# Kernel tuning notes

Measured on AMD Instinct MI355X. Metric: run time of the kernel, lower is better.

Reference implementation:

```python
import jax, jax.numpy as jnp
import numpy as np

B, L = 4, 1024
D_IN, D_MODEL, DEPTH = 8, 512, 4
D_INNER, D_STATE, D_CONV = 2 * D_MODEL, 16, 4
DT_RANK = (D_MODEL + 15) // 16  # 32


def setup_inputs():
    key = jax.random.key(0)
    ks = jax.random.split(key, 12)
    s = 0.02
    inp = {
        "x": jax.random.normal(ks[0], (B, L, D_IN), jnp.float32),
        "in_w": jax.random.normal(ks[1], (D_MODEL, D_IN), jnp.float32) * s,
        "in_b": jnp.zeros((D_MODEL,), jnp.float32),
        "W_xz": jax.random.normal(ks[2], (DEPTH, 2 * D_INNER, D_MODEL), jnp.float32) * s,
        "conv_w": jax.random.normal(ks[3], (DEPTH, D_INNER, D_CONV), jnp.float32) * 0.1,
        "conv_b": jnp.zeros((DEPTH, D_INNER), jnp.float32),
        "W_xp": jax.random.normal(ks[4], (DEPTH, DT_RANK + 2 * D_STATE, D_INNER), jnp.float32) * s,
        "W_dt": jax.random.normal(ks[5], (DEPTH, D_INNER, DT_RANK), jnp.float32) * 0.1,
        "b_dt": jax.random.uniform(ks[6], (DEPTH, D_INNER), jnp.float32, -4.0, -2.0),
        "A_log": jnp.broadcast_to(jnp.log(jnp.arange(1, D_STATE + 1, dtype=jnp.float32)), (DEPTH, D_INNER, D_STATE)) + 0.0,
        "D_param": jnp.ones((DEPTH, D_INNER), jnp.float32),
        "W_out": jax.random.normal(ks[7], (DEPTH, D_MODEL, D_INNER), jnp.float32) * s,
        "ln_g": jnp.ones((D_MODEL,), jnp.float32),
        "ln_b": jnp.zeros((D_MODEL,), jnp.float32),
    }
    return inp


def _silu(x):
    return x * jax.nn.sigmoid(x)


def _mamba_layer(h, Wxz, cw, cb, Wxp, Wdt, bdt, A_log, Dp, Wout):
    # in_proj -> (x, z)
    xz = jnp.einsum('bld,ed->ble', h, Wxz)           # (B,L,2*D_INNER)
    xc, z = jnp.split(xz, 2, axis=-1)
    # causal depthwise conv1d, kernel D_CONV
    xp = jnp.pad(xc, ((0, 0), (D_CONV - 1, 0), (0, 0)))
    xconv = sum(xp[:, k:k + L, :] * cw[:, k] for k in range(D_CONV)) + cb
    u = _silu(xconv)                                 # (B,L,D_INNER)
    # x_proj -> dt, B, C
    xdbl = jnp.einsum('bld,ed->ble', u, Wxp)
    dt_lr = xdbl[..., :DT_RANK]
    Bm = xdbl[..., DT_RANK:DT_RANK + D_STATE]        # (B,L,D_STATE)
    Cm = xdbl[..., DT_RANK + D_STATE:]               # (B,L,D_STATE)
    dt = jax.nn.softplus(jnp.einsum('blr,dr->bld', dt_lr, Wdt) + bdt)  # (B,L,D_INNER)
    A = -jnp.exp(A_log)                              # (D_INNER,D_STATE)

    def step(hst, inp):
        dt_t, B_t, C_t, u_t = inp                    # (B,Di),(B,S),(B,S),(B,Di)
        dA = jnp.exp(dt_t[..., None] * A)            # (B,Di,S)
        dBu = dt_t[..., None] * B_t[:, None, :] * u_t[..., None]
        hst = dA * hst + dBu
        y_t = jnp.einsum('bds,bs->bd', hst, C_t)
        return hst, y_t

    h0 = jnp.zeros((h.shape[0], D_INNER, D_STATE), h.dtype)
    xs = (dt.transpose(1, 0, 2), Bm.transpose(1, 0, 2), Cm.transpose(1, 0, 2), u.transpose(1, 0, 2))
    _, ys = jax.lax.scan(step, h0, xs)
    y = ys.transpose(1, 0, 2) + u * Dp               # (B,L,D_INNER)
    y = y * _silu(z)
    return jnp.einsum('ble,de->bld', y, Wout)


def reference(x, in_w, in_b, W_xz, conv_w, conv_b, W_xp, W_dt, b_dt, A_log, D_param, W_out, ln_g, ln_b):
    h = jnp.einsum('bli,di->bld', x, in_w) + in_b
    for i in range(DEPTH):
        h = _mamba_layer(h, W_xz[i], conv_w[i], conv_b[i], W_xp[i], W_dt[i], b_dt[i], A_log[i], D_param[i], W_out[i])
    mu = h.mean(-1, keepdims=True)
    var = ((h - mu) ** 2).mean(-1, keepdims=True)
    return (h - mu) * jax.lax.rsqrt(var + 1e-5) * ln_g + ln_b
```

## Files before the change

### kernel.cpp

```cpp
#include <hip/hip_runtime.h>
#include <math.h>

#define B_      4
#define L_      1024
#define D_INNC  8
#define DMODEL  512
#define DEPTH_  4
#define DINNER  1024
#define DSTATE  16
#define DCONV   4
#define DTRANK  32
#define MTOT    (B_*L_)
#define CHUNKS  32
#define CLEN    32

typedef float f32x4 __attribute__((ext_vector_type(4)));
typedef short s16x8 __attribute__((ext_vector_type(8)));
typedef unsigned short u16;
typedef unsigned short u16x4v __attribute__((ext_vector_type(4)));

__device__ __forceinline__ u16 f2bf(float v) {
    unsigned b = __float_as_uint(v);
    return (u16)((b + 0x7FFF + ((b >> 16) & 1)) >> 16);
}
__device__ __forceinline__ float bf2f(u16 h) {
    return __uint_as_float((unsigned)h << 16);
}

__global__ __launch_bounds__(256) void in_proj_kernel(
    const float* __restrict__ x, const float* __restrict__ w,
    const float* __restrict__ bias, u16* __restrict__ hb)
{
    int idx = blockIdx.x * 256 + threadIdx.x;
    int m = idx / DMODEL, d = idx % DMODEL;
    const float* xr = x + m * D_INNC;
    const float* wr = w + d * D_INNC;
    float acc = bias[d];
#pragma unroll
    for (int k = 0; k < D_INNC; ++k) acc += xr[k] * wr[k];
    hb[idx] = f2bf(acc);
}

__global__ __launch_bounds__(256) void wconv_kernel(
    const float* __restrict__ W, u16* __restrict__ Wb)
{
    int i = blockIdx.x * 256 + threadIdx.x;
    const float* src = W + (size_t)i * 8;
    float4 f0 = *(const float4*)src;
    float4 f1 = *(const float4*)(src + 4);
    float f[8] = {f0.x,f0.y,f0.z,f0.w,f1.x,f1.y,f1.z,f1.w};
    s16x8 hv;
#pragma unroll
    for (int e = 0; e < 8; ++e) hv[e] = (short)f2bf(f[e]);
    *(s16x8*)(Wb + (size_t)i * 8) = hv;
}

template<int BM, int BN, int MODE>
__global__ __launch_bounds__(256, 2) void gemm_bf16(
    const u16* __restrict__ A, int lda,
    const u16* __restrict__ B, int ldb,
    void* __restrict__ C0, void* __restrict__ C1,
    int ldc, int K)
{
    constexpr int FM  = BM / 32;
    constexpr int FN  = BN / 32;
    constexpr int ACH = BM / 64;
    constexpr int BCH = BN / 64;
    __shared__ __align__(16) u16 As[4*(BM+1)*8];
    __shared__ __align__(16) u16 Bs[4*(BN+1)*8];

    const int t    = threadIdx.x;
    const int lane = t & 63;
    const int w    = t >> 6;
    const int wm   = (w >> 1) * (BM / 2);
    const int wn   = (w & 1) * (BN / 2);
    const int quad = lane >> 4;
    const int l16  = lane & 15;
    const int m0   = blockIdx.y * BM;
    const int n0   = blockIdx.x * BN;

    f32x4 acc[FM][FN];
#pragma unroll
    for (int i = 0; i < FM; ++i)
#pragma unroll
        for (int j = 0; j < FN; ++j) acc[i][j] = (f32x4){0.f,0.f,0.f,0.f};

    s16x8 ra[ACH], rb[BCH];
#pragma unroll
    for (int c = 0; c < ACH; ++c) {
        int id = c*256 + t, row = id >> 2, kb = id & 3;
        ra[c] = *(const s16x8*)(A + (size_t)(m0 + row) * lda + kb*8);
    }
#pragma unroll
    for (int c = 0; c < BCH; ++c) {
        int id = c*256 + t, row = id >> 2, kb = id & 3;
        rb[c] = *(const s16x8*)(B + (size_t)(n0 + row) * ldb + kb*8);
    }

    for (int kk = 0; kk < K; kk += 32) {
        __syncthreads();
#pragma unroll
        for (int c = 0; c < ACH; ++c) {
            int id = c*256 + t, row = id >> 2, kb = id & 3;
            *(s16x8*)&As[(kb*(BM+1) + row) * 8] = ra[c];
        }
#pragma unroll
        for (int c = 0; c < BCH; ++c) {
            int id = c*256 + t, row = id >> 2, kb = id & 3;
            *(s16x8*)&Bs[(kb*(BN+1) + row) * 8] = rb[c];
        }
        __syncthreads();
        int kn = kk + 32;
        if (kn < K) {
#pragma unroll
            for (int c = 0; c < ACH; ++c) {
                int id = c*256 + t, row = id >> 2, kb = id & 3;
                ra[c] = *(const s16x8*)(A + (size_t)(m0 + row) * lda + kn + kb*8);
            }
#pragma unroll
            for (int c = 0; c < BCH; ++c) {
                int id = c*256 + t, row = id >> 2, kb = id & 3;
                rb[c] = *(const s16x8*)(B + (size_t)(n0 + row) * ldb + kn + kb*8);
            }
        }
        s16x8 afr[FM], bfr[FN];
#pragma unroll
        for (int i = 0; i < FM; ++i)
            afr[i] = *(const s16x8*)&As[(quad*(BM+1) + wm + i*16 + l16) * 8];
#pragma unroll
        for (int j = 0; j < FN; ++j)
            bfr[j] = *(const s16x8*)&Bs[(quad*(BN+1) + wn + j*16 + l16) * 8];
#pragma unroll
        for (int i = 0; i < FM; ++i)
#pragma unroll
            for (int j = 0; j < FN; ++j)
                acc[i][j] = __builtin_amdgcn_mfma_f32_16x16x32_bf16(afr[i], bfr[j], acc[i][j], 0, 0, 0);
    }

    if (MODE == 2) {
        u16* C = (u16*)C0;
#pragma unroll
        for (int i = 0; i < FM; ++i)
#pragma unroll
            for (int j = 0; j < FN; ++j) {
                int col = n0 + wn + j*16 + l16;
#pragma unroll
                for (int r = 0; r < 4; ++r) {
                    int row = m0 + wm + i*16 + quad*4 + r;
                    C[(size_t)row * ldc + col] = f2bf(acc[i][j][r]);
                }
            }
    } else if (MODE == 3) {
        u16*  dtlr = (u16*)C0;
        float* xd  = (float*)C1;
#pragma unroll
        for (int i = 0; i < FM; ++i)
#pragma unroll
            for (int j = 0; j < FN; ++j) {
                int col = n0 + wn + j*16 + l16;
#pragma unroll
                for (int r = 0; r < 4; ++r) {
                    int row = m0 + wm + i*16 + quad*4 + r;
                    float v = acc[i][j][r];
                    if (col < 32) dtlr[(size_t)row * 32 + col] = f2bf(v);
                    else          xd[(size_t)row * 64 + col]   = v;
                }
            }
    } else if (MODE == 4) {
        u16* dtb_ = (u16*)C0;
        const float* bdt = (const float*)C1;
#pragma unroll
        for (int i = 0; i < FM; ++i)
#pragma unroll
            for (int j = 0; j < FN; ++j) {
                int col = n0 + wn + j*16 + l16;
                float bb = bdt[col];
#pragma unroll
                for (int r = 0; r < 4; ++r) {
                    int row = m0 + wm + i*16 + quad*4 + r;
                    float v = acc[i][j][r] + bb;
                    float sp = (v > 20.f) ? v : log1pf(__expf(v));
                    dtb_[(size_t)row * ldc + col] = f2bf(sp);
                }
            }
    } else {
        u16* xcb = (u16*)C0;
        u16* szb = (u16*)C1;
#pragma unroll
        for (int i = 0; i < FM; ++i)
#pragma unroll
            for (int j = 0; j < FN; ++j) {
                int col = n0 + wn + j*16 + l16;
                bool isz = col >= DINNER;
                int cc = col & (DINNER - 1);
                u16* dst = isz ? szb : xcb;
#pragma unroll
                for (int r = 0; r < 4; ++r) {
                    int row = m0 + wm + i*16 + quad*4 + r;
                    float v = acc[i][j][r];
                    if (isz) v = v / (1.f + __expf(-v));
                    dst[(size_t)row * DINNER + cc] = f2bf(v);
                }
            }
    }
}

__global__ __launch_bounds__(256) void conv_silu_kernel(
    const u16* __restrict__ xcb, const float* __restrict__ cw,
    const float* __restrict__ cb, u16* __restrict__ ub)
{
    int idx = (blockIdx.x * 256 + threadIdx.x) * 2;
    int m = idx >> 10;
    int d = idx & (DINNER - 1);
    int l = m & (L_ - 1);

    const float4 w0 = *(const float4*)&cw[d * 4];
    const float4 w1 = *(const float4*)&cw[(d + 1) * 4];
    float a0 = cb[d], a1 = cb[d + 1];
#pragma unroll
    for (int k = 0; k < 4; ++k) {
        int lag = 3 - k;
        if (l >= lag) {
            unsigned v = *(const unsigned*)&xcb[(size_t)(m - lag) * DINNER + d];
            float x0 = bf2f((u16)(v & 0xffff));
            float x1 = bf2f((u16)(v >> 16));
            float wk0 = (&w0.x)[k], wk1 = (&w1.x)[k];
            a0 += x0 * wk0; a1 += x1 * wk1;
        }
    }
    a0 = a0 / (1.f + __expf(-a0));
    a1 = a1 / (1.f + __expf(-a1));
    unsigned pack = (unsigned)f2bf(a0) | ((unsigned)f2bf(a1) << 16);
    *(unsigned*)&ub[idx] = pack;
}

__global__ __launch_bounds__(256) void scan1_kernel(
    const u16* __restrict__ ub, const float* xdbl,
    const u16* __restrict__ dtb, const float* __restrict__ A_log,
    u16* __restrict__ hfinal, float* dtsum_out)
{
    __shared__ float Bs[CLEN][16];
    const int blk  = blockIdx.x;
    const int dblk = blk & 3;
    const int c    = (blk >> 2) & (CHUNKS - 1);
    const int b    = blk >> 7;
    const int d    = dblk * 256 + threadIdx.x;
    const int mbase = b * L_ + c * CLEN;

#pragma unroll
    for (int q = 0; q < 2; ++q) {
        int idx = q * 256 + threadIdx.x;
        int tt = idx >> 4, ss = idx & 15;
        Bs[tt][ss] = xdbl[(size_t)(mbase + tt) * 64 + 32 + ss];
    }
    float A[16];
    {
        float4 a4[4];
#pragma unroll
        for (int q = 0; q < 4; ++q) a4[q] = *(const float4*)&A_log[d * 16 + q * 4];
        const float* af = (const float*)a4;
#pragma unroll
        for (int s = 0; s < 16; ++s) A[s] = -__expf(af[s]);
    }
    __syncthreads();

    float h[16];
#pragma unroll
    for (int s = 0; s < 16; ++s) h[s] = 0.f;
    float dts = 0.f;

    for (int t0 = 0; t0 < CLEN; t0 += 8) {
        float dt8[8], u8[8];
#pragma unroll
        for (int j = 0; j < 8; ++j) {
            int m = mbase + t0 + j;
            dt8[j] = bf2f(dtb[(size_t)m * DINNER + d]);
            u8[j]  = bf2f(ub [(size_t)m * DINNER + d]);
        }
#pragma unroll
        for (int j = 0; j < 8; ++j) {
            float dtv = dt8[j], dtu = dtv * u8[j];
            dts += dtv;
            float Bt[16];
#pragma unroll
            for (int q = 0; q < 4; ++q)
                *(float4*)&Bt[q*4] = *(const float4*)&Bs[t0 + j][q*4];
#pragma unroll
            for (int s = 0; s < 16; ++s) {
                float dA = __expf(dtv * A[s]);
                h[s] = dA * h[s] + dtu * Bt[s];
            }
        }
    }
    size_t base = ((size_t)(b * CHUNKS + c) * DINNER + d) * 16;
    s16x8 p0, p1;
#pragma unroll
    for (int s = 0; s < 8; ++s) { p0[s] = (short)f2bf(h[s]); p1[s] = (short)f2bf(h[s+8]); }
    *(s16x8*)&hfinal[base]     = p0;
    *(s16x8*)&hfinal[base + 8] = p1;
    int i = (b * CHUNKS + c) * DINNER + d;
    dtsum_out[(i >> 5) * 64 + (i & 31)] = dts;
}

__global__ __launch_bounds__(256) void scan2_kernel(
    u16* __restrict__ hfinal, const float* __restrict__ dtsum,
    const float* __restrict__ A_log)
{
    int t = blockIdx.x * 256 + threadIdx.x;
    int s = t & 15, d = (t >> 4) & (DINNER - 1), b = t >> 14;
    float As = -__expf(A_log[d * DSTATE + s]);
    float h = 0.f;
    for (int c0 = 0; c0 < CHUNKS; c0 += 8) {
        float hf8[8], dts8[8];
#pragma unroll
        for (int j = 0; j < 8; ++j) {
            int c = c0 + j;
            int i = (b * CHUNKS + c) * DINNER + d;
            dts8[j] = dtsum[(i >> 5) * 64 + (i & 31)];
            hf8[j]  = bf2f(hfinal[((size_t)i) * 16 + s]);
        }
#pragma unroll
        for (int j = 0; j < 8; ++j) {
            int c = c0 + j;
            size_t idx = ((size_t)((b * CHUNKS + c) * DINNER + d)) * 16 + s;
            hfinal[idx] = f2bf(h);
            h = __expf(As * dts8[j]) * h + hf8[j];
        }
    }
}

__global__ __launch_bounds__(256) void scan3_kernel(
    const u16* __restrict__ szb, const u16* __restrict__ ub,
    const float* xdbl, const u16* __restrict__ dtb,
    const float* __restrict__ A_log, const float* __restrict__ Dp,
    const u16* __restrict__ hstart, u16* __restrict__ yb)
{
    __shared__ float Bs[CLEN][16];
    __shared__ float Cs[CLEN][16];
    const int blk  = blockIdx.x;
    const int dblk = blk & 3;
    const int c    = (blk >> 2) & (CHUNKS - 1);
    const int b    = blk >> 7;
    const int d    = dblk * 256 + threadIdx.x;
    const int mbase = b * L_ + c * CLEN;

#pragma unroll
    for (int q = 0; q < 2; ++q) {
        int idx = q * 256 + threadIdx.x;
        int tt = idx >> 4, ss = idx & 15;
        Bs[tt][ss] = xdbl[(size_t)(mbase + tt) * 64 + 32 + ss];
        Cs[tt][ss] = xdbl[(size_t)(mbase + tt) * 64 + 48 + ss];
    }
    float A[16];
    {
        float4 a4[4];
#pragma unroll
        for (int q = 0; q < 4; ++q) a4[q] = *(const float4*)&A_log[d * 16 + q * 4];
        const float* af = (const float*)a4;
#pragma unroll
        for (int s = 0; s < 16; ++s) A[s] = -__expf(af[s]);
    }
    const float Dval = Dp[d];

    float h[16];
    {
        size_t base = ((size_t)(b * CHUNKS + c) * DINNER + d) * 16;
        s16x8 p0 = *(const s16x8*)&hstart[base];
        s16x8 p1 = *(const s16x8*)&hstart[base + 8];
#pragma unroll
        for (int s = 0; s < 8; ++s) { h[s] = bf2f((u16)p0[s]); h[s+8] = bf2f((u16)p1[s]); }
    }
    __syncthreads();

    for (int t0 = 0; t0 < CLEN; t0 += 8) {
        float dt8[8], u8[8], sz8[8];
#pragma unroll
        for (int j = 0; j < 8; ++j) {
            int m = mbase + t0 + j;
            dt8[j] = bf2f(dtb[(size_t)m * DINNER + d]);
            u8[j]  = bf2f(ub [(size_t)m * DINNER + d]);
            sz8[j] = bf2f(szb[(size_t)m * DINNER + d]);
        }
#pragma unroll
        for (int j = 0; j < 8; ++j) {
            float dtv = dt8[j], dtu = dtv * u8[j];
            float Bt[16], Ct[16];
#pragma unroll
            for (int q = 0; q < 4; ++q) {
                *(float4*)&Bt[q*4] = *(const float4*)&Bs[t0 + j][q*4];
                *(float4*)&Ct[q*4] = *(const float4*)&Cs[t0 + j][q*4];
            }
            float yv = 0.f;
#pragma unroll
            for (int s = 0; s < 16; ++s) {
                float dA = __expf(dtv * A[s]);
                h[s] = dA * h[s] + dtu * Bt[s];
                yv += h[s] * Ct[s];
            }
            int m = mbase + t0 + j;
            yb[(size_t)m * DINNER + d] = f2bf((yv + u8[j] * Dval) * sz8[j]);
        }
    }
}

__global__ __launch_bounds__(256) void ln_kernel(
    const u16* __restrict__ hb, const float* __restrict__ g,
    const float* __restrict__ bta, float* __restrict__ out)
{
    int m = blockIdx.x;
    size_t base = (size_t)m * DMODEL;
    int t = threadIdx.x;
    float v0 = bf2f(hb[base + t]);
    float v1 = bf2f(hb[base + t + 256]);
    float sum = v0 + v1, sq = v0*v0 + v1*v1;
#pragma unroll
    for (int off = 32; off; off >>= 1) {
        sum += __shfl_down(sum, off);
        sq  += __shfl_down(sq,  off);
    }
    __shared__ float ls[4], lq[4];
    int w = t >> 6;
    if ((t & 63) == 0) { ls[w] = sum; lq[w] = sq; }
    __syncthreads();
    sum = ls[0] + ls[1] + ls[2] + ls[3];
    sq  = lq[0] + lq[1] + lq[2] + lq[3];
    float mu  = sum * (1.f / DMODEL);
    float var = sq * (1.f / DMODEL) - mu * mu;
    float rs  = rsqrtf(var + 1e-5f);
    out[base + t]       = (v0 - mu) * rs * g[t]       + bta[t];
    out[base + t + 256] = (v1 - mu) * rs * g[t + 256] + bta[t + 256];
}

extern "C" void kernel_launch(void* const* d_in, const int* in_sizes, int n_in,
                              void* d_out, int out_size, void* d_ws, size_t ws_size,
                              hipStream_t stream)
{
    const float* x      = (const float*)d_in[0];
    const float* in_w   = (const float*)d_in[1];
    const float* in_b   = (const float*)d_in[2];
    const float* W_xz   = (const float*)d_in[3];
    const float* conv_w = (const float*)d_in[4];
    const float* conv_b = (const float*)d_in[5];
    const float* W_xp   = (const float*)d_in[6];
    const float* W_dt   = (const float*)d_in[7];
    const float* b_dt   = (const float*)d_in[8];
    const float* A_log  = (const float*)d_in[9];
    const float* D_par  = (const float*)d_in[10];
    const float* W_out  = (const float*)d_in[11];
    const float* ln_g   = (const float*)d_in[12];
    const float* ln_b   = (const float*)d_in[13];
    float* out = (float*)d_out;

    float* ws      = (float*)d_ws;
    float* hbF     = ws;
    float* hfinF   = hbF    + 1048576;
    float* xcbF    = hfinF  + 1048576;
    float* szbF    = xcbF   + 2097152;
    float* ubF     = szbF   + 2097152;
    float* xdbl    = ubF    + 2097152;
    float* dtbF    = xdbl   + 262144;
    float* ybF     = dtbF   + 2097152;
    float* wxzF    = ybF    + 2097152;
    float* woutF   = wxzF   + 2097152;
    float* wxpF    = woutF  + 1048576;
    float* wdtF    = wxpF   + 131072;
    float* dtlrF   = wdtF   + 65536;

    u16* hb     = (u16*)hbF;
    u16* hfinal = (u16*)hfinF;
    u16* xcb  = (u16*)xcbF;
    u16* szb  = (u16*)szbF;
    u16* ub   = (u16*)ubF;
    u16* dtb  = (u16*)dtbF;
    u16* yb   = (u16*)ybF;
    u16* wxzb  = (u16*)wxzF;
    u16* woutb = (u16*)woutF;
    u16* wxpb  = (u16*)wxpF;
    u16* wdtb  = (u16*)wdtF;
    u16* dtlrb = (u16*)dtlrF;

    wconv_kernel<<<(DEPTH_*2048*DMODEL/8)/256, 256, 0, stream>>>(W_xz, wxzb);
    wconv_kernel<<<(DEPTH_*DMODEL*DINNER/8)/256, 256, 0, stream>>>(W_out, woutb);
    wconv_kernel<<<(DEPTH_*64*DINNER/8)/256, 256, 0, stream>>>(W_xp, wxpb);
    wconv_kernel<<<(DEPTH_*DINNER*DTRANK/8)/256, 256, 0, stream>>>(W_dt, wdtb);

    in_proj_kernel<<<MTOT*DMODEL/256, 256, 0, stream>>>(x, in_w, in_b, hb);

    for (int layer = 0; layer < DEPTH_; ++layer) {
        const float* cw    = conv_w + (size_t)layer * DINNER * DCONV;
        const float* cb    = conv_b + (size_t)layer * DINNER;
        const float* bdt   = b_dt   + (size_t)layer * DINNER;
        const float* Alog  = A_log  + (size_t)layer * DINNER * DSTATE;
        const float* Dp    = D_par  + (size_t)layer * DINNER;
        const u16* wxzL    = wxzb  + (size_t)layer * 2048 * DMODEL;
        const u16* woutL   = woutb + (size_t)layer * DMODEL * DINNER;
        const u16* wxpL    = wxpb  + (size_t)layer * 64 * DINNER;
        const u16* wdtL    = wdtb  + (size_t)layer * DINNER * DTRANK;

        gemm_bf16<128,128,1><<<dim3(2048/128, MTOT/128), 256, 0, stream>>>(
            hb, DMODEL, wxzL, DMODEL, xcb, szb, 0, DMODEL);
        conv_silu_kernel<<<MTOT*DINNER/2/256, 256, 0, stream>>>(xcb, cw, cb, ub);
        gemm_bf16<64,64,3><<<dim3(1, MTOT/64), 256, 0, stream>>>(
            ub, DINNER, wxpL, DINNER, dtlrb, xdbl, 0, DINNER);
        gemm_bf16<64,64,4><<<dim3(DINNER/64, MTOT/64), 256, 0, stream>>>(
            dtlrb, DTRANK, wdtL, DTRANK, dtb, (void*)bdt, DINNER, DTRANK);
        scan1_kernel<<<B_*CHUNKS*(DINNER/256), 256, 0, stream>>>(ub, xdbl, dtb, Alog, hfinal, xdbl);
        scan2_kernel<<<(B_*DINNER*DSTATE)/256, 256, 0, stream>>>(hfinal, xdbl, Alog);
        scan3_kernel<<<B_*CHUNKS*(DINNER/256), 256, 0, stream>>>(szb, ub, xdbl, dtb, Alog, Dp, hfinal, yb);
        gemm_bf16<64,64,2><<<dim3(DMODEL/64, MTOT/64), 256, 0, stream>>>(
            yb, DINNER, woutL, DINNER, hb, nullptr, DMODEL, DINNER);
    }

    ln_kernel<<<MTOT, 256, 0, stream>>>(hb, ln_g, ln_b, out);
}
```

Before: 608.0 us.

## Fuse dt projection into x_proj GEMM epilogue and halve scan chunk length

The x_proj GEMM now keeps the dt low-rank slice in shared memory and immediately runs the W_dt projection with MFMA plus softplus in its epilogue. This removes the separate dt GEMM launch and the dtlr round trip through global memory. The scan chunking changes from 32 chunks of 32 to 64 chunks of 16, which doubles the scan1/scan3 grid for more parallelism but lengthens the sequential chunk carry in scan2 and doubles the hfinal buffer. Chunk dt sums move to their own dense buffer instead of being interleaved into xdbl.

```diff
diff --git a/kernel.cpp b/kernel.cpp
--- a/kernel.cpp
+++ b/kernel.cpp
@@ -11,8 +11,8 @@
 #define DCONV   4
 #define DTRANK  32
 #define MTOT    (B_*L_)
-#define CHUNKS  32
-#define CLEN    32
+#define CHUNKS  64
+#define CLEN    16
 
 typedef float f32x4 __attribute__((ext_vector_type(4)));
 typedef short s16x8 __attribute__((ext_vector_type(8)));
@@ -60,7 +60,8 @@
     const u16* __restrict__ A, int lda,
     const u16* __restrict__ B, int ldb,
     void* __restrict__ C0, void* __restrict__ C1,
-    int ldc, int K)
+    int ldc, int K,
+    const u16* __restrict__ W2, const float* __restrict__ bias2)
 {
     constexpr int FM  = BM / 32;
     constexpr int FN  = BN / 32;
@@ -137,7 +138,7 @@
                 acc[i][j] = __builtin_amdgcn_mfma_f32_16x16x32_bf16(afr[i], bfr[j], acc[i][j], 0, 0, 0);
     }
 
-    if (MODE == 2) {
+    if constexpr (MODE == 2) {
         u16* C = (u16*)C0;
 #pragma unroll
         for (int i = 0; i < FM; ++i)
@@ -150,39 +151,58 @@
                     C[(size_t)row * ldc + col] = f2bf(acc[i][j][r]);
                 }
             }
-    } else if (MODE == 3) {
-        u16*  dtlr = (u16*)C0;
-        float* xd  = (float*)C1;
-#pragma unroll
-        for (int i = 0; i < FM; ++i)
-#pragma unroll
-            for (int j = 0; j < FN; ++j) {
-                int col = n0 + wn + j*16 + l16;
+    } else if constexpr (MODE == 5) {
+        __shared__ __align__(16) u16 dl[64 * 40];
+        float* xd = (float*)C1;
+        if (wn == 0) {
+#pragma unroll
+            for (int i = 0; i < FM; ++i)
+#pragma unroll
+                for (int j = 0; j < FN; ++j) {
+                    int col = j*16 + l16;
+#pragma unroll
+                    for (int r = 0; r < 4; ++r) {
+                        int row = wm + i*16 + quad*4 + r;
+                        dl[row*40 + col] = f2bf(acc[i][j][r]);
+                    }
+                }
+        } else {
+#pragma unroll
+            for (int i = 0; i < FM; ++i)
+#pragma unroll
+                for (int j = 0; j < FN; ++j) {
+                    int col = 32 + j*16 + l16;
+#pragma unroll
+                    for (int r = 0; r < 4; ++r) {
+                        int row = m0 + wm + i*16 + quad*4 + r;
+                        xd[(size_t)row * 64 + col] = acc[i][j][r];
+                    }
+                }
+        }
+        __syncthreads();
+        s16x8 da[4];
+#pragma unroll
+        for (int i = 0; i < 4; ++i)
+            da[i] = *(const s16x8*)&dl[(i*16 + l16)*40 + quad*8];
+        u16* dtb_ = (u16*)C0;
+        const int nb0 = w * 256;
+#pragma unroll
+        for (int jj = 0; jj < 16; ++jj) {
+            int n = nb0 + jj*16 + l16;
+            s16x8 db = *(const s16x8*)(W2 + (size_t)n * DTRANK + quad*8);
+            float bb = bias2[n];
+#pragma unroll
+            for (int i = 0; i < 4; ++i) {
+                f32x4 dacc = (f32x4){0.f,0.f,0.f,0.f};
+                dacc = __builtin_amdgcn_mfma_f32_16x16x32_bf16(da[i], db, dacc, 0, 0, 0);
 #pragma unroll
                 for (int r = 0; r < 4; ++r) {
-                    int row = m0 + wm + i*16 + quad*4 + r;
-                    float v = acc[i][j][r];
-                    if (col < 32) dtlr[(size_t)row * 32 + col] = f2bf(v);
-                    else          xd[(size_t)row * 64 + col]   = v;
+                    float v = dacc[r] + bb;
+                    float sp = (v > 20.f) ? v : log1pf(__expf(v));
+                    dtb_[(size_t)(m0 + i*16 + quad*4 + r) * DINNER + n] = f2bf(sp);
                 }
             }
-    } else if (MODE == 4) {
-        u16* dtb_ = (u16*)C0;
-        const float* bdt = (const float*)C1;
-#pragma unroll
-        for (int i = 0; i < FM; ++i)
-#pragma unroll
-            for (int j = 0; j < FN; ++j) {
-                int col = n0 + wn + j*16 + l16;
-                float bb = bdt[col];
-#pragma unroll
-                for (int r = 0; r < 4; ++r) {
-                    int row = m0 + wm + i*16 + quad*4 + r;
-                    float v = acc[i][j][r] + bb;
-                    float sp = (v > 20.f) ? v : log1pf(__expf(v));
-                    dtb_[(size_t)row * ldc + col] = f2bf(sp);
-                }
-            }
+        }
     } else {
         u16* xcb = (u16*)C0;
         u16* szb = (u16*)C1;
@@ -237,19 +257,18 @@
 __global__ __launch_bounds__(256) void scan1_kernel(
     const u16* __restrict__ ub, const float* xdbl,
     const u16* __restrict__ dtb, const float* __restrict__ A_log,
-    u16* __restrict__ hfinal, float* dtsum_out)
+    u16* __restrict__ hfinal, float* __restrict__ dsum)
 {
     __shared__ float Bs[CLEN][16];
     const int blk  = blockIdx.x;
     const int dblk = blk & 3;
     const int c    = (blk >> 2) & (CHUNKS - 1);
-    const int b    = blk >> 7;
+    const int b    = blk >> 8;
     const int d    = dblk * 256 + threadIdx.x;
     const int mbase = b * L_ + c * CLEN;
 
-#pragma unroll
-    for (int q = 0; q < 2; ++q) {
-        int idx = q * 256 + threadIdx.x;
+    {
+        int idx = threadIdx.x;
         int tt = idx >> 4, ss = idx & 15;
         Bs[tt][ss] = xdbl[(size_t)(mbase + tt) * 64 + 32 + ss];
     }
@@ -298,12 +317,11 @@
     for (int s = 0; s < 8; ++s) { p0[s] = (short)f2bf(h[s]); p1[s] = (short)f2bf(h[s+8]); }
     *(s16x8*)&hfinal[base]     = p0;
     *(s16x8*)&hfinal[base + 8] = p1;
-    int i = (b * CHUNKS + c) * DINNER + d;
-    dtsum_out[(i >> 5) * 64 + (i & 31)] = dts;
+    dsum[(size_t)(b * CHUNKS + c) * DINNER + d] = dts;
 }
 
 __global__ __launch_bounds__(256) void scan2_kernel(
-    u16* __restrict__ hfinal, const float* __restrict__ dtsum,
+    u16* __restrict__ hfinal, const float* __restrict__ dsum,
     const float* __restrict__ A_log)
 {
     int t = blockIdx.x * 256 + threadIdx.x;
@@ -315,14 +333,14 @@
 #pragma unroll
         for (int j = 0; j < 8; ++j) {
             int c = c0 + j;
-            int i = (b * CHUNKS + c) * DINNER + d;
-            dts8[j] = dtsum[(i >> 5) * 64 + (i & 31)];
-            hf8[j]  = bf2f(hfinal[((size_t)i) * 16 + s]);
+            size_t i = (size_t)(b * CHUNKS + c) * DINNER + d;
+            dts8[j] = dsum[i];
+            hf8[j]  = bf2f(hfinal[i * 16 + s]);
         }
 #pragma unroll
         for (int j = 0; j < 8; ++j) {
             int c = c0 + j;
-            size_t idx = ((size_t)((b * CHUNKS + c) * DINNER + d)) * 16 + s;
+            size_t idx = ((size_t)(b * CHUNKS + c) * DINNER + d) * 16 + s;
             hfinal[idx] = f2bf(h);
             h = __expf(As * dts8[j]) * h + hf8[j];
         }
@@ -340,13 +358,12 @@
     const int blk  = blockIdx.x;
     const int dblk = blk & 3;
     const int c    = (blk >> 2) & (CHUNKS - 1);
-    const int b    = blk >> 7;
+    const int b    = blk >> 8;
     const int d    = dblk * 256 + threadIdx.x;
     const int mbase = b * L_ + c * CLEN;
 
-#pragma unroll
-    for (int q = 0; q < 2; ++q) {
-        int idx = q * 256 + threadIdx.x;
+    {
+        int idx = threadIdx.x;
         int tt = idx >> 4, ss = idx & 15;
         Bs[tt][ss] = xdbl[(size_t)(mbase + tt) * 64 + 32 + ss];
         Cs[tt][ss] = xdbl[(size_t)(mbase + tt) * 64 + 48 + ss];
@@ -454,7 +471,7 @@
     float* ws      = (float*)d_ws;
     float* hbF     = ws;
     float* hfinF   = hbF    + 1048576;
-    float* xcbF    = hfinF  + 1048576;
+    float* xcbF    = hfinF  + 2097152;
     float* szbF    = xcbF   + 2097152;
     float* ubF     = szbF   + 2097152;
     float* xdbl    = ubF    + 2097152;
@@ -464,7 +481,7 @@
     float* woutF   = wxzF   + 2097152;
     float* wxpF    = woutF  + 1048576;
     float* wdtF    = wxpF   + 131072;
-    float* dtlrF   = wdtF   + 65536;
+    float* dsum    = wdtF   + 65536;
 
     u16* hb     = (u16*)hbF;
     u16* hfinal = (u16*)hfinF;
@@ -477,7 +494,6 @@
     u16* woutb = (u16*)woutF;
     u16* wxpb  = (u16*)wxpF;
     u16* wdtb  = (u16*)wdtF;
-    u16* dtlrb = (u16*)dtlrF;
 
     wconv_kernel<<<(DEPTH_*2048*DMODEL/8)/256, 256, 0, stream>>>(W_xz, wxzb);
     wconv_kernel<<<(DEPTH_*DMODEL*DINNER/8)/256, 256, 0, stream>>>(W_out, woutb);
@@ -498,17 +514,15 @@
         const u16* wdtL    = wdtb  + (size_t)layer * DINNER * DTRANK;
 
         gemm_bf16<128,128,1><<<dim3(2048/128, MTOT/128), 256, 0, stream>>>(
-            hb, DMODEL, wxzL, DMODEL, xcb, szb, 0, DMODEL);
+            hb, DMODEL, wxzL, DMODEL, xcb, szb, 0, DMODEL, nullptr, nullptr);
         conv_silu_kernel<<<MTOT*DINNER/2/256, 256, 0, stream>>>(xcb, cw, cb, ub);
-        gemm_bf16<64,64,3><<<dim3(1, MTOT/64), 256, 0, stream>>>(
-            ub, DINNER, wxpL, DINNER, dtlrb, xdbl, 0, DINNER);
-        gemm_bf16<64,64,4><<<dim3(DINNER/64, MTOT/64), 256, 0, stream>>>(
-            dtlrb, DTRANK, wdtL, DTRANK, dtb, (void*)bdt, DINNER, DTRANK);
-        scan1_kernel<<<B_*CHUNKS*(DINNER/256), 256, 0, stream>>>(ub, xdbl, dtb, Alog, hfinal, xdbl);
-        scan2_kernel<<<(B_*DINNER*DSTATE)/256, 256, 0, stream>>>(hfinal, xdbl, Alog);
+        gemm_bf16<64,64,5><<<dim3(1, MTOT/64), 256, 0, stream>>>(
+            ub, DINNER, wxpL, DINNER, dtb, xdbl, 0, DINNER, wdtL, bdt);
+        scan1_kernel<<<B_*CHUNKS*(DINNER/256), 256, 0, stream>>>(ub, xdbl, dtb, Alog, hfinal, dsum);
+        scan2_kernel<<<(B_*DINNER*DSTATE)/256, 256, 0, stream>>>(hfinal, dsum, Alog);
         scan3_kernel<<<B_*CHUNKS*(DINNER/256), 256, 0, stream>>>(szb, ub, xdbl, dtb, Alog, Dp, hfinal, yb);
         gemm_bf16<64,64,2><<<dim3(DMODEL/64, MTOT/64), 256, 0, stream>>>(
-            yb, DINNER, woutL, DINNER, hb, nullptr, DMODEL, DINNER);
+            yb, DINNER, woutL, DINNER, hb, nullptr, DMODEL, DINNER, nullptr, nullptr);
     }
 
     ln_kernel<<<MTOT, 256, 0, stream>>>(hb, ln_g, ln_b, out);
```

Result: slower. 892.8 us (+46.8%).
